# Performance work log

Hardware: AMD Instinct MI355X
Metric: run time of the kernel (lower is better)

Reference implementation:

```python
import jax, jax.numpy as jnp
import numpy as np

N_NODES = 10000
N_EDGES = 640000
F_NODE = 128   # n_node_features
F_EDGE = 128   # hiddens (edge_attr width)


def setup_inputs() -> dict:
    key = jax.random.key(0)
    k1, k2, k3, k4 = jax.random.split(key, 4)
    x = jax.random.normal(k1, (N_NODES, F_NODE), dtype=jnp.float32)
    edge_index = jax.random.randint(k2, (2, N_EDGES), 0, N_NODES, dtype=jnp.int64)
    edge_attr = jax.random.normal(k3, (N_EDGES, F_EDGE), dtype=jnp.float32)
    u = jax.random.normal(k4, (1, 16), dtype=jnp.float32)
    batch = jnp.zeros((N_NODES,), dtype=jnp.int64)
    return {"x": x, "edge_index": edge_index, "edge_attr": edge_attr, "u": u, "batch": batch}


def reference(x, edge_index, edge_attr, u, batch):
    # row: destination (scatter target), col: source (gather index)
    row, col = edge_index[0], edge_index[1]
    n = x.shape[0]
    # [E, F_NODE + F_EDGE]: gather source node feats, concat edge feats
    msg = jnp.concatenate([x[col], edge_attr], axis=1)
    # scatter_mean over destination nodes (count clamped to 1, matching torch_scatter)
    summed = jax.ops.segment_sum(msg, row, num_segments=n)
    counts = jax.ops.segment_sum(jnp.ones((row.shape[0],), x.dtype), row, num_segments=n)
    mean = summed / jnp.maximum(counts, 1.0)[:, None]
    # [N, 2*F_NODE + F_EDGE]
    return jnp.concatenate([x, mean], axis=1)
```

## Files before the change

kernel.cpp:

```cpp
#include <hip/hip_runtime.h>
#include <hip/hip_bf16.h>

#define F_NODE 128
#define F_EDGE 128
#define OUT_W  384

__global__ void count_kernel(const int* __restrict__ row, int* __restrict__ counts, int E) {
    int e = blockIdx.x * blockDim.x + threadIdx.x;
    if (e < E) atomicAdd(&counts[row[e]], 1);
}

__global__ __launch_bounds__(256) void scan_kernel(const int* __restrict__ counts,
                                                   int* __restrict__ offsets,
                                                   int* __restrict__ cursor, int n) {
    const int t = threadIdx.x;
    const int chunk = (n + 255) / 256;
    const int lo = t * chunk;
    const int hi = min(lo + chunk, n);

    int local = 0;
    for (int i = lo; i < hi; ++i) local += counts[i];

    const int lane = t & 63, wv = t >> 6;
    int incl = local;
    for (int d = 1; d < 64; d <<= 1) {
        int v = __shfl_up(incl, d);
        if (lane >= d) incl += v;
    }
    __shared__ int wsum[4];
    if (lane == 63) wsum[wv] = incl;
    __syncthreads();
    int wpre = 0;
    for (int w = 0; w < wv; ++w) wpre += wsum[w];
    int run = wpre + incl - local;

    for (int i = lo; i < hi; ++i) {
        offsets[i] = run;
        cursor[i]  = run;
        run += counts[i];
    }
    if (t == 255) offsets[n] = wpre + incl;
}

__global__ void scatter_kernel(const int* __restrict__ row, const int* __restrict__ col,
                               int* __restrict__ cursor, int2* __restrict__ pairs, int E) {
    int e = blockIdx.x * blockDim.x + threadIdx.x;
    if (e < E) {
        int r = row[e];
        int c = col[e];
        int pos = atomicAdd(&cursor[r], 1);
        pairs[pos] = make_int2(e, c);
    }
}

__global__ __launch_bounds__(256) void aggregate_kernel(
    const float* __restrict__ x, const float* __restrict__ edge_attr,
    const int* __restrict__ offsets, const int2* __restrict__ pairs,
    float* __restrict__ out, int n_nodes) {

    const int wave = threadIdx.x >> 6;
    const int lane = threadIdx.x & 63;
    const int node = blockIdx.x * 4 + wave;
    if (node >= n_nodes) return;

    const int start = offsets[node];
    const int end   = offsets[node + 1];
    const int cnt   = end - start;

    const bool is_x = lane < 32;
    const int  sub4 = (is_x ? lane : (lane - 32)) * 4;

    float4 sum = make_float4(0.f, 0.f, 0.f, 0.f);

    for (int base = start; base < end; base += 64) {
        const int m = min(64, end - base);
        int idx = base + lane;
        if (idx >= end) idx = end - 1;
        const int2 pr = pairs[idx];
        for (int i = 0; i < m; ++i) {
            const int e = __shfl(pr.x, i);
            const int c = __shfl(pr.y, i);
            const float* px = x         + (size_t)c * F_NODE;
            const float* pe = edge_attr + (size_t)e * F_EDGE;
            const float* p  = (is_x ? px : pe) + sub4;
            const float4 v = *(const float4*)p;
            sum.x += v.x; sum.y += v.y; sum.z += v.z; sum.w += v.w;
        }
    }

    const float inv = 1.0f / fmaxf((float)cnt, 1.0f);
    float* orow = out + (size_t)node * OUT_W;

    float4 mean = make_float4(sum.x * inv, sum.y * inv, sum.z * inv, sum.w * inv);
    *(float4*)(orow + F_NODE + lane * 4) = mean;

    const float* xr = x + (size_t)node * F_NODE;
    *(float2*)(orow + lane * 2) = *(const float2*)(xr + lane * 2);
}

extern "C" void kernel_launch(void* const* d_in, const int* in_sizes, int n_in,
                              void* d_out, int out_size, void* d_ws, size_t ws_size,
                              hipStream_t stream) {
    const float* x          = (const float*)d_in[0];
    const int*   edge_index = (const int*)d_in[1];
    const float* edge_attr  = (const float*)d_in[2];

    const int n_nodes = in_sizes[0] / F_NODE;
    const int E       = in_sizes[1] / 2;
    const int* row = edge_index;
    const int* col = edge_index + E;

    int2* pairs   = (int2*)d_ws;
    int*  counts  = (int*)(pairs + E);
    int*  offsets = counts + n_nodes;
    int*  cursor  = offsets + n_nodes + 1;

    float* out = (float*)d_out;

    hipMemsetAsync(counts, 0, (size_t)n_nodes * sizeof(int), stream);

    const int TB = 256;
    count_kernel<<<(E + TB - 1) / TB, TB, 0, stream>>>(row, counts, E);
    scan_kernel<<<1, 256, 0, stream>>>(counts, offsets, cursor, n_nodes);
    scatter_kernel<<<(E + TB - 1) / TB, TB, 0, stream>>>(row, col, cursor, pairs, E);
    aggregate_kernel<<<(n_nodes + 3) / 4, 256, 0, stream>>>(x, edge_attr, offsets,
                                                            pairs, out, n_nodes);
}
```

Baseline: 584.9 us.

## Build CSR with per-block shared-memory histograms and split aggregation across two waves

The global-atomic counting and scatter are replaced by a per-block histogram in shared memory, a column-sum totals pass, a scan, per-block start offsets and a shared-atomic scatter into separate edge-id and column-id arrays. The goal is to cut global atomic contention when building the CSR. Aggregation now uses two waves per node, one summing x rows and one summing edge_attr rows, each handling two edges per iteration with half-waves. edge_attr is read with nontemporal loads. This adds kernel launches and a 128xN histogram buffer in workspace.

```diff
diff --git a/kernel.cpp b/kernel.cpp
--- a/kernel.cpp
+++ b/kernel.cpp
@@ -1,101 +1,161 @@
 #include <hip/hip_runtime.h>
-#include <hip/hip_bf16.h>
 
-#define F_NODE 128
-#define F_EDGE 128
+#define F      128
 #define OUT_W  384
+#define NBLK   128
+#define HT     512
 
-__global__ void count_kernel(const int* __restrict__ row, int* __restrict__ counts, int E) {
-    int e = blockIdx.x * blockDim.x + threadIdx.x;
-    if (e < E) atomicAdd(&counts[row[e]], 1);
+typedef __attribute__((ext_vector_type(4))) float f4;
+
+__global__ __launch_bounds__(HT) void hist_kernel(const int* __restrict__ row,
+                                                  int* __restrict__ hist,
+                                                  int E, int N, int chunk) {
+    extern __shared__ int h[];
+    const int t = threadIdx.x;
+    for (int i = t; i < N; i += HT) h[i] = 0;
+    __syncthreads();
+    const int lo = blockIdx.x * chunk;
+    const int hi = min(lo + chunk, E);
+    for (int i = lo + t; i < hi; i += HT) atomicAdd(&h[row[i]], 1);
+    __syncthreads();
+    int* dst = hist + (size_t)blockIdx.x * N;
+    for (int i = t; i < N; i += HT) dst[i] = h[i];
 }
 
-__global__ __launch_bounds__(256) void scan_kernel(const int* __restrict__ counts,
-                                                   int* __restrict__ offsets,
-                                                   int* __restrict__ cursor, int n) {
+__global__ void totals_kernel(const int* __restrict__ hist, int* __restrict__ tot, int N) {
+    const int n = blockIdx.x * blockDim.x + threadIdx.x;
+    if (n >= N) return;
+    int s = 0;
+    for (int b = 0; b < NBLK; ++b) s += hist[(size_t)b * N + n];
+    tot[n] = s;
+}
+
+__global__ __launch_bounds__(1024) void scan_kernel(const int* __restrict__ tot,
+                                                    int* __restrict__ offsets, int N) {
     const int t = threadIdx.x;
-    const int chunk = (n + 255) / 256;
-    const int lo = t * chunk;
-    const int hi = min(lo + chunk, n);
-
+    const int chunk = (N + 1023) / 1024;
+    const int lo = min(t * chunk, N);
+    const int hi = min(lo + chunk, N);
     int local = 0;
-    for (int i = lo; i < hi; ++i) local += counts[i];
-
+    for (int i = lo; i < hi; ++i) local += tot[i];
     const int lane = t & 63, wv = t >> 6;
     int incl = local;
     for (int d = 1; d < 64; d <<= 1) {
         int v = __shfl_up(incl, d);
         if (lane >= d) incl += v;
     }
-    __shared__ int wsum[4];
+    __shared__ int wsum[16];
     if (lane == 63) wsum[wv] = incl;
     __syncthreads();
     int wpre = 0;
     for (int w = 0; w < wv; ++w) wpre += wsum[w];
     int run = wpre + incl - local;
-
-    for (int i = lo; i < hi; ++i) {
-        offsets[i] = run;
-        cursor[i]  = run;
-        run += counts[i];
-    }
-    if (t == 255) offsets[n] = wpre + incl;
+    for (int i = lo; i < hi; ++i) { offsets[i] = run; run += tot[i]; }
+    if (t == 1023) offsets[N] = wpre + incl;
 }
 
-__global__ void scatter_kernel(const int* __restrict__ row, const int* __restrict__ col,
-                               int* __restrict__ cursor, int2* __restrict__ pairs, int E) {
-    int e = blockIdx.x * blockDim.x + threadIdx.x;
-    if (e < E) {
-        int r = row[e];
-        int c = col[e];
-        int pos = atomicAdd(&cursor[r], 1);
-        pairs[pos] = make_int2(e, c);
+__global__ void blockstart_kernel(int* hist, const int* __restrict__ offsets, int N) {
+    const int n = blockIdx.x * blockDim.x + threadIdx.x;
+    if (n >= N) return;
+    int run = offsets[n];
+    for (int b = 0; b < NBLK; ++b) {
+        const size_t k = (size_t)b * N + n;
+        const int v = hist[k];
+        hist[k] = run;
+        run += v;
+    }
+}
+
+__global__ __launch_bounds__(HT) void scatter_kernel(const int* __restrict__ row,
+                                                     const int* __restrict__ col,
+                                                     const int* __restrict__ hist,
+                                                     int* __restrict__ eid,
+                                                     int* __restrict__ cid,
+                                                     int E, int N, int chunk) {
+    extern __shared__ int cur[];
+    const int t = threadIdx.x;
+    const int* src = hist + (size_t)blockIdx.x * N;
+    for (int i = t; i < N; i += HT) cur[i] = src[i];
+    __syncthreads();
+    const int lo = blockIdx.x * chunk;
+    const int hi = min(lo + chunk, E);
+    for (int i = lo + t; i < hi; i += HT) {
+        const int r = row[i];
+        const int p = atomicAdd(&cur[r], 1);
+        eid[p] = i;
+        cid[p] = col[i];
+    }
+}
+
+template <bool NT>
+__device__ __forceinline__ void accum_half(const float* __restrict__ mat,
+                                           const int* __restrict__ list,
+                                           int start, int end, int lane, f4& acc) {
+    const int which = lane >> 5;
+    const int sub   = lane & 31;
+    for (int base = start; base < end; base += 64) {
+        const int m = min(64, end - base);
+        int idx = base + lane;
+        if (idx >= end) idx = end - 1;
+        const int myid = list[idx];
+        const int full = m & ~1;
+        for (int i = 0; i < full; i += 2) {
+            const int id = __shfl(myid, i + which);
+            const f4* p = (const f4*)(mat + (size_t)id * F + sub * 4);
+            const f4 v = NT ? __builtin_nontemporal_load(p) : *p;
+            acc += v;
+        }
+        if (m & 1) {
+            const int id = __shfl(myid, full);
+            if (which == 0) {
+                const f4* p = (const f4*)(mat + (size_t)id * F + sub * 4);
+                const f4 v = NT ? __builtin_nontemporal_load(p) : *p;
+                acc += v;
+            }
+        }
     }
 }
 
 __global__ __launch_bounds__(256) void aggregate_kernel(
     const float* __restrict__ x, const float* __restrict__ edge_attr,
-    const int* __restrict__ offsets, const int2* __restrict__ pairs,
-    float* __restrict__ out, int n_nodes) {
+    const int* __restrict__ offsets, const int* __restrict__ eid,
+    const int* __restrict__ cid, float* __restrict__ out, int N) {
 
     const int wave = threadIdx.x >> 6;
     const int lane = threadIdx.x & 63;
-    const int node = blockIdx.x * 4 + wave;
-    if (node >= n_nodes) return;
+    const int wid  = blockIdx.x * 4 + wave;
+    const int node = wid >> 1;
+    const int half = wid & 1;
+    if (node >= N) return;
 
     const int start = offsets[node];
     const int end   = offsets[node + 1];
-    const int cnt   = end - start;
 
-    const bool is_x = lane < 32;
-    const int  sub4 = (is_x ? lane : (lane - 32)) * 4;
+    f4 acc = {0.f, 0.f, 0.f, 0.f};
+    if (half == 0) accum_half<false>(x,         cid, start, end, lane, acc);
+    else           accum_half<true >(edge_attr, eid, start, end, lane, acc);
 
-    float4 sum = make_float4(0.f, 0.f, 0.f, 0.f);
+    acc.x += __shfl_xor(acc.x, 32);
+    acc.y += __shfl_xor(acc.y, 32);
+    acc.z += __shfl_xor(acc.z, 32);
+    acc.w += __shfl_xor(acc.w, 32);
 
-    for (int base = start; base < end; base += 64) {
-        const int m = min(64, end - base);
-        int idx = base + lane;
-        if (idx >= end) idx = end - 1;
-        const int2 pr = pairs[idx];
-        for (int i = 0; i < m; ++i) {
-            const int e = __shfl(pr.x, i);
-            const int c = __shfl(pr.y, i);
-            const float* px = x         + (size_t)c * F_NODE;
-            const float* pe = edge_attr + (size_t)e * F_EDGE;
-            const float* p  = (is_x ? px : pe) + sub4;
-            const float4 v = *(const float4*)p;
-            sum.x += v.x; sum.y += v.y; sum.z += v.z; sum.w += v.w;
-        }
-    }
-
-    const float inv = 1.0f / fmaxf((float)cnt, 1.0f);
+    const float inv = 1.0f / fmaxf((float)(end - start), 1.0f);
+    const int which = lane >> 5, sub = lane & 31;
     float* orow = out + (size_t)node * OUT_W;
 
-    float4 mean = make_float4(sum.x * inv, sum.y * inv, sum.z * inv, sum.w * inv);
-    *(float4*)(orow + F_NODE + lane * 4) = mean;
-
-    const float* xr = x + (size_t)node * F_NODE;
-    *(float2*)(orow + lane * 2) = *(const float2*)(xr + lane * 2);
+    if (half == 0) {
+        if (which == 0) {
+            f4 mean = {acc.x * inv, acc.y * inv, acc.z * inv, acc.w * inv};
+            *(f4*)(orow + F + sub * 4) = mean;
+        } else {
+            *(f4*)(orow + sub * 4) =
+                *(const f4*)(x + (size_t)node * F + sub * 4);
+        }
+    } else if (which == 0) {
+        f4 mean = {acc.x * inv, acc.y * inv, acc.z * inv, acc.w * inv};
+        *(f4*)(orow + 2 * F + sub * 4) = mean;
+    }
 }
 
 extern "C" void kernel_launch(void* const* d_in, const int* in_sizes, int n_in,
@@ -105,24 +165,27 @@
     const int*   edge_index = (const int*)d_in[1];
     const float* edge_attr  = (const float*)d_in[2];
 
-    const int n_nodes = in_sizes[0] / F_NODE;
-    const int E       = in_sizes[1] / 2;
+    const int N = in_sizes[0] / F;
+    const int E = in_sizes[1] / 2;
     const int* row = edge_index;
     const int* col = edge_index + E;
 
-    int2* pairs   = (int2*)d_ws;
-    int*  counts  = (int*)(pairs + E);
-    int*  offsets = counts + n_nodes;
-    int*  cursor  = offsets + n_nodes + 1;
+    int* hist    = (int*)d_ws;
+    int* tot     = hist + (size_t)NBLK * N;
+    int* offsets = tot + N;
+    int* eid     = offsets + N + 1;
+    int* cid     = eid + E;
 
     float* out = (float*)d_out;
 
-    hipMemsetAsync(counts, 0, (size_t)n_nodes * sizeof(int), stream);
+    const int chunk  = (E + NBLK - 1) / NBLK;
+    const size_t smem = (size_t)N * sizeof(int);
 
-    const int TB = 256;
-    count_kernel<<<(E + TB - 1) / TB, TB, 0, stream>>>(row, counts, E);
-    scan_kernel<<<1, 256, 0, stream>>>(counts, offsets, cursor, n_nodes);
-    scatter_kernel<<<(E + TB - 1) / TB, TB, 0, stream>>>(row, col, cursor, pairs, E);
-    aggregate_kernel<<<(n_nodes + 3) / 4, 256, 0, stream>>>(x, edge_attr, offsets,
-                                                            pairs, out, n_nodes);
+    hist_kernel      <<<NBLK, HT, smem, stream>>>(row, hist, E, N, chunk);
+    totals_kernel    <<<(N + 255) / 256, 256, 0, stream>>>(hist, tot, N);
+    scan_kernel      <<<1, 1024, 0, stream>>>(tot, offsets, N);
+    blockstart_kernel<<<(N + 255) / 256, 256, 0, stream>>>(hist, offsets, N);
+    scatter_kernel   <<<NBLK, HT, smem, stream>>>(row, col, hist, eid, cid, E, N, chunk);
+    aggregate_kernel <<<(2 * N + 3) / 4, 256, 0, stream>>>(x, edge_attr, offsets,
+                                                           eid, cid, out, N);
 }
```

After: 512.3 us. 1.14x faster.
